# Kernel optimization log

Hardware: AMD Instinct MI355X
Metric: run time of the kernel (lower is better)

Reference implementation:

```python
import jax, jax.numpy as jnp
import numpy as np

B, A, T, H, E, O, TY, SC, AG = 8, 64, 12, 128, 128, 128, 8, 32, 16


def setup_inputs() -> dict:
    ks = jax.random.split(jax.random.key(0), 32)

    def rn(k, shape, s=1.0):
        return jax.random.normal(k, shape, dtype=jnp.float32) * s

    z = lambda *s: jnp.zeros(s, dtype=jnp.float32)
    return {
        "trajectories": rn(ks[0], (B, A, T, 3)),
        "normalized_trajectories": rn(ks[1], (B, A, T, 3)),
        "agent_type": rn(ks[2], (B, A, TY)),
        "scene_data": rn(ks[3], (B, T, SC)),
        "agent_data": rn(ks[4], (B, A, T, AG)),
        "relevant_agents": jnp.ones((B, A), dtype=jnp.float32),
        "W_in": rn(ks[5], (6, H), 0.05), "b_in": z(H),
        "W_node_type": rn(ks[6], (TY, H), 0.05), "b_node_type": z(H),
        "W_agent": rn(ks[7], (AG, H), 0.05), "b_agent": z(H),
        "W_scene": rn(ks[8], (SC, H), 0.05), "b_scene": z(H),
        "W_edge_in": rn(ks[9], (2 * 6 + 2 * TY, E), 0.05), "b_edge_in": z(E),
        "W_edge_type": rn(ks[10], (2 * TY, E), 0.05), "b_edge_type": z(E),
        "W_edge": rn(ks[11], (2 * H + E, E), 0.05), "b_edge": z(E),
        "W_self": rn(ks[12], (H + E + TY, E), 0.05), "b_self": z(E),
        "W_e2n": rn(ks[13], (E, H), 0.05), "b_e2n": z(H),
        "W_ih": rn(ks[14], (5 * H, 4 * H), 0.05),
        "W_hh": rn(ks[15], (H, 4 * H), 0.05),
        "b_ih": z(4 * H), "b_hh": z(4 * H),
        "W_pred": rn(ks[16], (H, O), 0.05), "b_pred": z(O),
    }


def reference(trajectories, normalized_trajectories, agent_type, scene_data, agent_data,
              relevant_agents, W_in, b_in, W_node_type, b_node_type, W_agent, b_agent,
              W_scene, b_scene, W_edge_in, b_edge_in, W_edge_type, b_edge_type,
              W_edge, b_edge, W_self, b_self, W_e2n, b_e2n,
              W_ih, W_hh, b_ih, b_hh, W_pred, b_pred):
    # cat(normalized, raw) along last dim -> 2*(input_dim+1)=6
    both = jnp.concatenate([normalized_trajectories, trajectories], axis=-1)  # [B,A,T,6]
    coord = jax.nn.relu(both @ W_in + b_in)                                   # [B,A,T,H]
    type_enc = agent_type @ W_node_type + b_node_type                          # [B,A,H]
    agent_enc = (agent_data @ W_agent + b_agent) * relevant_agents[:, :, None, None]  # [B,A,T,H]
    scene_enc = scene_data @ W_scene + b_scene                                 # [B,T,H]

    b, a, t_steps = both.shape[0], both.shape[1], both.shape[2]
    Hd = W_in.shape[1]
    Ed = W_edge.shape[1]
    ty = agent_type.shape[-1]

    # initial pairwise edge states from agent features at t=0 + type-pair encoding
    ty_i = jnp.broadcast_to(agent_type[:, :, None, :], (b, a, a, ty))
    ty_j = jnp.broadcast_to(agent_type[:, None, :, :], (b, a, a, ty))
    ty_pair = jnp.concatenate([ty_i, ty_j], axis=-1)                           # [B,A,A,2*TY]
    f0 = both[:, :, 0, :]                                                      # [B,A,6]
    f_i = jnp.broadcast_to(f0[:, :, None, :], (b, a, a, f0.shape[-1]))
    f_j = jnp.broadcast_to(f0[:, None, :, :], (b, a, a, f0.shape[-1]))
    edge0 = (jnp.concatenate([f_i, f_j, ty_pair], axis=-1) @ W_edge_in + b_edge_in
             + ty_pair @ W_edge_type + b_edge_type)                            # [B,A,A,E]

    h0 = jnp.zeros((b, a, Hd), both.dtype)
    c0 = jnp.zeros((b, a, Hd), both.dtype)
    se0 = jnp.zeros((b, a, Ed), both.dtype)

    def step(carry, xs):
        h, c, es, se = carry
        coord_t, scene_t, agent_t, t = xs
        # edge MLP on gathered node pairs (BN is identity in eval, dropout off)
        hi = jnp.broadcast_to(h[:, :, None, :], (b, a, a, Hd))
        hj = jnp.broadcast_to(h[:, None, :, :], (b, a, a, Hd))
        es_new = jnp.concatenate([hi, hj, es], axis=-1) @ W_edge + b_edge      # [B,A,A,E]
        se_new = jnp.concatenate([h, se, agent_type], axis=-1) @ W_self + b_self  # [B,A,E]
        agg = es_new.sum(axis=2) + se_new                                      # scatter-sum to nodes
        node_edges = (agg @ W_e2n + b_e2n) * (t > 0).astype(h.dtype)           # zeros at t==0
        x = jnp.concatenate(
            [coord_t, type_enc, node_edges,
             jnp.broadcast_to(scene_t[:, None, :], (b, a, Hd)), agent_t], axis=-1)  # [B,A,5H]
        gates = x @ W_ih + h @ W_hh + b_ih + b_hh
        gi, gf, gg, go = jnp.split(gates, 4, axis=-1)
        c_new = jax.nn.sigmoid(gf) * c + jax.nn.sigmoid(gi) * jnp.tanh(gg)
        h_new = jax.nn.sigmoid(go) * jnp.tanh(c_new)
        out = jax.nn.relu(h_new @ W_pred + b_pred)                             # layer_pred
        return (h_new, c_new, es_new, se_new), out

    xs = (jnp.moveaxis(coord, 2, 0), jnp.moveaxis(scene_enc, 1, 0),
          jnp.moveaxis(agent_enc, 2, 0), jnp.arange(t_steps))
    _, ys = jax.lax.scan(step, (h0, c0, edge0, se0), xs)                       # ys: [T,B,A,O]
    return jnp.moveaxis(ys, 0, 2)                                              # [B,A,T,O]
```

## Files before the change

kernel.cpp:

```cpp
#include <hip/hip_runtime.h>

constexpr int NB = 8, NA = 64, NT = 12, NH = 128, NTY = 8, NSC = 32, NAG = 16;

struct Params {
    const float *traj, *ntraj, *ty, *sd, *adata, *rel;
    const float *W_in, *b_in, *W_nt, *b_nt, *W_ag, *b_ag, *W_sc, *b_sc;
    const float *W_ein, *b_ein, *W_ety, *b_ety;
    const float *W_edge, *b_edge, *W_self, *b_self, *W_e2n, *b_e2n;
    const float *W_ih, *W_hh, *b_ih, *b_hh, *W_pred, *b_pred;
    float *h0, *h1, *c, *se, *R;
    float *Wty, *Wsc, *Wag, *Wcomb, *vbase, *vag, *vbe, *sesty, *Xs, *hall, *out;
};

__global__ __launch_bounds__(512) void k_fold(Params p) {
    const int blk = blockIdx.x, c = threadIdx.x;
    __shared__ float lrow[NH];
    __shared__ float b1[NH], b2[NH], b3[NH], b4[NH];
    if (blk < 184) {
        const float* src; int ihoff, row; float* dst;
        if (blk < 8)       { row = blk;      src = p.W_nt  + row * NH; ihoff = 128; dst = p.Wty; }
        else if (blk < 40) { row = blk - 8;  src = p.W_sc  + row * NH; ihoff = 384; dst = p.Wsc; }
        else if (blk < 56) { row = blk - 40; src = p.W_ag  + row * NH; ihoff = 512; dst = p.Wag; }
        else               { row = blk - 56; src = p.W_e2n + row * NH; ihoff = 256; dst = p.Wcomb; }
        if (c < NH) lrow[c] = src[c];
        __syncthreads();
        float acc = 0.f;
        for (int k = 0; k < NH; ++k) acc += lrow[k] * p.W_ih[(ihoff + k) * 512 + c];
        dst[row * 512 + c] = acc;
    } else {
        if (c < NH) { b1[c] = p.b_nt[c]; b2[c] = p.b_sc[c]; b3[c] = p.b_ag[c]; b4[c] = p.b_e2n[c]; }
        __syncthreads();
        float vb = p.b_ih[c] + p.b_hh[c], va = 0.f, ve = 0.f;
        for (int k = 0; k < NH; ++k) {
            vb += b1[k] * p.W_ih[(128 + k) * 512 + c] + b2[k] * p.W_ih[(384 + k) * 512 + c];
            va += b3[k] * p.W_ih[(512 + k) * 512 + c];
            ve += b4[k] * p.W_ih[(256 + k) * 512 + c];
        }
        p.vbase[c] = vb; p.vag[c] = va; p.vbe[c] = ve;
    }
}

__global__ void k_r0(Params p) {
    const int row = blockIdx.x, n = threadIdx.x;
    const int b = row / NA, i = row % NA;
    __shared__ float lf[NA][6];
    __shared__ float lt[NA][NTY];
    __shared__ float sumf[6], sumt[NTY];
    if (threadIdx.x < NA) {
        int j = threadIdx.x, rj = b * NA + j;
        for (int k = 0; k < 3; ++k) {
            lf[j][k]     = p.ntraj[(rj * NT + 0) * 3 + k];
            lf[j][3 + k] = p.traj [(rj * NT + 0) * 3 + k];
        }
        for (int k = 0; k < NTY; ++k) lt[j][k] = p.ty[rj * NTY + k];
    }
    __syncthreads();
    if (threadIdx.x < 6) {
        float s = 0.f; for (int j = 0; j < NA; ++j) s += lf[j][threadIdx.x];
        sumf[threadIdx.x] = s;
    } else if (threadIdx.x < 6 + NTY) {
        int k = threadIdx.x - 6; float s = 0.f;
        for (int j = 0; j < NA; ++j) s += lt[j][k];
        sumt[k] = s;
    }
    __syncthreads();
    float acc_i = p.b_ein[n] + p.b_ety[n];
    for (int k = 0; k < 6; ++k)   acc_i += lf[i][k] * p.W_ein[k * NH + n];
    for (int k = 0; k < NTY; ++k) acc_i += lt[i][k] * (p.W_ein[(12 + k) * NH + n] + p.W_ety[k * NH + n]);
    float acc_j = 0.f;
    for (int k = 0; k < 6; ++k)   acc_j += sumf[k] * p.W_ein[(6 + k) * NH + n];
    for (int k = 0; k < NTY; ++k) acc_j += sumt[k] * (p.W_ein[(20 + k) * NH + n] + p.W_ety[(NTY + k) * NH + n]);
    p.R[row * NH + n] = 64.f * acc_i + acc_j;
    float sv = p.b_self[n];
    for (int k = 0; k < NTY; ++k) sv += lt[i][k] * p.W_self[(2 * NH + k) * NH + n];
    p.sesty[row * NH + n] = sv;
}

__global__ __launch_bounds__(512) void k_xstatic(Params p) {
    const int g = blockIdx.x, tid = threadIdx.x, b = g >> 6;
    __shared__ float coordL[NT][NH];
    __shared__ float sceneL[NT][NSC];
    __shared__ float agentL[NT][NAG];
    __shared__ float tyL[NTY];
    const float relv = p.rel[g];
    for (int idx = tid; idx < NT * NH; idx += 512) {
        int r = idx >> 7, k = idx & 127;
        float acc = p.b_in[k];
        const float* nt = p.ntraj + (g * NT + r) * 3;
        const float* tr = p.traj  + (g * NT + r) * 3;
        for (int j = 0; j < 3; ++j) acc += nt[j] * p.W_in[j * NH + k] + tr[j] * p.W_in[(3 + j) * NH + k];
        coordL[r][k] = fmaxf(acc, 0.f);
    }
    for (int i = tid; i < NT * NSC; i += 512) { int r = i >> 5, k = i & 31; sceneL[r][k] = p.sd[(b * NT + r) * NSC + k]; }
    for (int i = tid; i < NT * NAG; i += 512) { int r = i >> 4, k = i & 15; agentL[r][k] = p.adata[(g * NT + r) * NAG + k] * relv; }
    if (tid < NTY) tyL[tid] = p.ty[g * NTY + tid];
    __syncthreads();
    const int c = tid;
    float base = p.vbase[c] + relv * p.vag[c];
    for (int i = 0; i < NTY; ++i) base += tyL[i] * p.Wty[i * 512 + c];
    const float vbeL = p.vbe[c];
    float acc[NT];
#pragma unroll
    for (int r = 0; r < NT; ++r) acc[r] = base + (r > 0 ? vbeL : 0.f);
    for (int k = 0; k < NH; ++k) { float w = p.W_ih[k * 512 + c];
#pragma unroll
        for (int r = 0; r < NT; ++r) acc[r] += coordL[r][k] * w; }
    for (int k = 0; k < NSC; ++k) { float w = p.Wsc[k * 512 + c];
#pragma unroll
        for (int r = 0; r < NT; ++r) acc[r] += sceneL[r][k] * w; }
    for (int k = 0; k < NAG; ++k) { float w = p.Wag[k * 512 + c];
#pragma unroll
        for (int r = 0; r < NT; ++r) acc[r] += agentL[r][k] * w; }
#pragma unroll
    for (int r = 0; r < NT; ++r) p.Xs[((size_t)(g * NT + r)) * 512 + c] = acc[r];
}

__global__ __launch_bounds__(1024) void k_step(Params p, int t) {
    const int tid = threadIdx.x;
    const int r0 = blockIdx.x * 2;
    const int b = r0 >> 6;
    const int n = tid & 127;
    const int g8 = tid >> 7;
    const float* __restrict__ hcur = (t & 1) ? p.h1 : p.h0;
    float* hnxt = (t & 1) ? p.h0 : p.h1;

    __shared__ float lh[2][NH], lR[2][NH], lse[2][NH];
    __shared__ float ps[16][NH];
    __shared__ float hsumL[NH], shw2[NH];
    __shared__ float lagg[2][NH];
    __shared__ float lgp[2][2][512];

    if (tid < 256) {
        int rr = tid >> 7, k = tid & 127;
        lh[rr][k]  = hcur[(r0 + rr) * NH + k];
        lR[rr][k]  = p.R [(r0 + rr) * NH + k];
        lse[rr][k] = p.se[(r0 + rr) * NH + k];
    }
    if (t > 0) {
        float s = 0.f;
        const float* hb = hcur + (b * NA + g8 * 8) * NH + n;
#pragma unroll
        for (int j = 0; j < 8; ++j) s += hb[j * NH];
        ps[g8][n] = s;
    }
    __syncthreads();
    if (t > 0 && tid < NH) {
        float s = 0.f;
#pragma unroll
        for (int q = 0; q < 8; ++q) s += ps[q][tid];
        hsumL[tid] = s;
    }
    __syncthreads();
    if (t > 0) {
        float s = 0.f;
        const float* w2 = p.W_edge + NH * NH + n;
#pragma unroll
        for (int k = 16 * g8; k < 16 * g8 + 16; ++k) s += hsumL[k] * w2[k * NH];
        ps[g8][n] = s;
    }
    __syncthreads();
    if (tid < NH) {
        float s = 0.f;
        if (t > 0) {
#pragma unroll
            for (int q = 0; q < 8; ++q) s += ps[q][tid];
        }
        shw2[tid] = s;
    }
    __syncthreads();

    {
        const int path = g8 >> 1, kh = g8 & 1;
        const float* wb; const float* d0; const float* d1;
        if (path == 0)      { wb = p.W_edge + n;               d0 = lh[0];  d1 = lh[1];  }
        else if (path == 1) { wb = p.W_edge + 2 * NH * NH + n; d0 = lR[0];  d1 = lR[1];  }
        else if (path == 2) { wb = p.W_self + n;               d0 = lh[0];  d1 = lh[1];  }
        else                { wb = p.W_self + NH * NH + n;     d0 = lse[0]; d1 = lse[1]; }
        float a0 = 0.f, a1 = 0.f;
#pragma unroll 8
        for (int k = 64 * kh; k < 64 * kh + 64; ++k) {
            float w = wb[k * NH];
            a0 += d0[k] * w; a1 += d1[k] * w;
        }
        ps[g8 * 2 + 0][n] = a0;
        ps[g8 * 2 + 1][n] = a1;
    }
    __syncthreads();
    if (tid < 256) {
        int rr = tid >> 7, k = tid & 127;
        float a1v = ps[0 + rr][k] + ps[2 + rr][k];
        float a3v = ps[4 + rr][k] + ps[6 + rr][k];
        float aSv = ps[8 + rr][k] + ps[10 + rr][k]
                  + ps[12 + rr][k] + ps[14 + rr][k];
        float Rn = 64.f * a1v + shw2[k] + a3v + 64.f * p.b_edge[k];
        float Sn = aSv + p.sesty[(r0 + rr) * NH + k];
        p.R [(r0 + rr) * NH + k] = Rn;
        p.se[(r0 + rr) * NH + k] = Sn;
        lagg[rr][k] = Rn + Sn;
    }
    __syncthreads();

    {
        const int c = tid & 511, kh2 = tid >> 9;
        float a0 = 0.f, a1v = 0.f;
        if (kh2 == 0) {
            a0  = p.Xs[((size_t)r0 * NT + t) * 512 + c];
            a1v = p.Xs[((size_t)(r0 + 1) * NT + t) * 512 + c];
        }
        if (t > 0) {
            const float* wc = p.Wcomb + c;
            const float* wh = p.W_hh + c;
#pragma unroll 8
            for (int k = 64 * kh2; k < 64 * kh2 + 64; ++k) {
                float w = wc[k * 512];
                a0 += lagg[0][k] * w; a1v += lagg[1][k] * w;
            }
#pragma unroll 8
            for (int k = 64 * kh2; k < 64 * kh2 + 64; ++k) {
                float w = wh[k * 512];
                a0 += lh[0][k] * w; a1v += lh[1][k] * w;
            }
        }
        lgp[kh2][0][c] = a0;
        lgp[kh2][1][c] = a1v;
    }
    __syncthreads();

    if (tid < 256) {
        const int rr = tid >> 7, k = tid & 127, g = r0 + rr;
        float gi = lgp[0][rr][k]          + lgp[1][rr][k];
        float gf = lgp[0][rr][NH + k]     + lgp[1][rr][NH + k];
        float gg = lgp[0][rr][2 * NH + k] + lgp[1][rr][2 * NH + k];
        float go = lgp[0][rr][3 * NH + k] + lgp[1][rr][3 * NH + k];
        float si = 1.f / (1.f + expf(-gi));
        float sf = 1.f / (1.f + expf(-gf));
        float so = 1.f / (1.f + expf(-go));
        float cn = sf * p.c[g * NH + k] + si * tanhf(gg);
        float hn = so * tanhf(cn);
        p.c[g * NH + k] = cn;
        hnxt[g * NH + k] = hn;
        p.hall[((size_t)g * NT + t) * NH + k] = hn;
    }
}

__global__ void k_out(Params p) {
    const int row0 = blockIdx.x * 8, tid = threadIdx.x;
    __shared__ float lhL[8][NH];
    for (int idx = tid; idx < 8 * NH; idx += 256) {
        int r = idx >> 7, k = idx & 127;
        lhL[r][k] = p.hall[((size_t)(row0 + r)) * NH + k];
    }
    __syncthreads();
    const int n = tid & 127, half = tid >> 7, rb = half * 4;
    float a0 = p.b_pred[n], a1 = a0, a2 = a0, a3 = a0;
    for (int k = 0; k < NH; ++k) {
        float w = p.W_pred[k * NH + n];
        a0 += lhL[rb][k] * w; a1 += lhL[rb + 1][k] * w;
        a2 += lhL[rb + 2][k] * w; a3 += lhL[rb + 3][k] * w;
    }
    p.out[((size_t)(row0 + rb))     * NH + n] = fmaxf(a0, 0.f);
    p.out[((size_t)(row0 + rb + 1)) * NH + n] = fmaxf(a1, 0.f);
    p.out[((size_t)(row0 + rb + 2)) * NH + n] = fmaxf(a2, 0.f);
    p.out[((size_t)(row0 + rb + 3)) * NH + n] = fmaxf(a3, 0.f);
}

extern "C" void kernel_launch(void* const* d_in, const int* in_sizes, int n_in,
                              void* d_out, int out_size, void* d_ws, size_t ws_size,
                              hipStream_t stream) {
    const float* const* in = (const float* const*)d_in;
    Params p;
    p.traj = in[0]; p.ntraj = in[1]; p.ty = in[2]; p.sd = in[3]; p.adata = in[4]; p.rel = in[5];
    p.W_in = in[6]; p.b_in = in[7]; p.W_nt = in[8]; p.b_nt = in[9];
    p.W_ag = in[10]; p.b_ag = in[11]; p.W_sc = in[12]; p.b_sc = in[13];
    p.W_ein = in[14]; p.b_ein = in[15]; p.W_ety = in[16]; p.b_ety = in[17];
    p.W_edge = in[18]; p.b_edge = in[19]; p.W_self = in[20]; p.b_self = in[21];
    p.W_e2n = in[22]; p.b_e2n = in[23];
    p.W_ih = in[24]; p.W_hh = in[25]; p.b_ih = in[26]; p.b_hh = in[27];
    p.W_pred = in[28]; p.b_pred = in[29];

    float* ws = (float*)d_ws;
    const size_t S = (size_t)NB * NA * NH;
    p.h0 = ws;
    p.h1 = ws + S;
    p.c  = ws + 2 * S;
    p.se = ws + 3 * S;
    p.R  = ws + 4 * S;
    float* w = ws + 5 * S;
    p.Wty   = w;              w += 8 * 512;
    p.Wsc   = w;              w += 32 * 512;
    p.Wag   = w;              w += 16 * 512;
    p.Wcomb = w;              w += 128 * 512;
    p.vbase = w;              w += 512;
    p.vag   = w;              w += 512;
    p.vbe   = w;              w += 512;
    p.sesty = w;              w += (size_t)NB * NA * NH;
    p.Xs    = w;              w += (size_t)NB * NA * NT * 512;
    p.hall  = w;              w += (size_t)NB * NA * NT * NH;
    p.out = (float*)d_out;

    hipMemsetAsync(p.h0, 0, 4 * S * sizeof(float), stream);
    k_fold<<<185, 512, 0, stream>>>(p);
    k_r0<<<NB * NA, 128, 0, stream>>>(p);
    k_xstatic<<<NB * NA, 512, 0, stream>>>(p);
    for (int t = 0; t < NT; ++t)
        k_step<<<NB * NA / 2, 1024, 0, stream>>>(p, t);
    k_out<<<NB * NA * NT / 8, 256, 0, stream>>>(p);
}
```

Measured before the change: 192.6 us.

## Fuse prelude kernels, process four rows per step block, fold output projection into step

Merges the weight-folding and edge-init kernels into one prelude launch. Each recurrent step block now handles four agent rows instead of two, so each weight load feeds twice as many rows. The prediction layer moves into the step kernel, which removes the hall buffer and the separate output kernel. The cost is half as many step blocks, which means less parallelism across the GPU, plus a longer serial matvec loop per thread.

```diff
diff --git a/kernel.cpp b/kernel.cpp
--- a/kernel.cpp
+++ b/kernel.cpp
@@ -9,71 +9,74 @@
     const float *W_edge, *b_edge, *W_self, *b_self, *W_e2n, *b_e2n;
     const float *W_ih, *W_hh, *b_ih, *b_hh, *W_pred, *b_pred;
     float *h0, *h1, *c, *se, *R;
-    float *Wty, *Wsc, *Wag, *Wcomb, *vbase, *vag, *vbe, *sesty, *Xs, *hall, *out;
+    float *Wty, *Wsc, *Wag, *Wcomb, *vbase, *vag, *vbe, *sesty, *Xs, *out;
 };
 
-__global__ __launch_bounds__(512) void k_fold(Params p) {
-    const int blk = blockIdx.x, c = threadIdx.x;
-    __shared__ float lrow[NH];
-    __shared__ float b1[NH], b2[NH], b3[NH], b4[NH];
-    if (blk < 184) {
-        const float* src; int ihoff, row; float* dst;
-        if (blk < 8)       { row = blk;      src = p.W_nt  + row * NH; ihoff = 128; dst = p.Wty; }
-        else if (blk < 40) { row = blk - 8;  src = p.W_sc  + row * NH; ihoff = 384; dst = p.Wsc; }
-        else if (blk < 56) { row = blk - 40; src = p.W_ag  + row * NH; ihoff = 512; dst = p.Wag; }
-        else               { row = blk - 56; src = p.W_e2n + row * NH; ihoff = 256; dst = p.Wcomb; }
-        if (c < NH) lrow[c] = src[c];
+__global__ __launch_bounds__(512) void k_prelude(Params p) {
+    const int blk = blockIdx.x, tid = threadIdx.x;
+    if (blk < 185) {
+        const int c = tid;
+        __shared__ float lrow[NH];
+        __shared__ float b1[NH], b2[NH], b3[NH], b4[NH];
+        if (blk < 184) {
+            const float* src; int ihoff, row; float* dst;
+            if (blk < 8)       { row = blk;      src = p.W_nt  + row * NH; ihoff = 128; dst = p.Wty; }
+            else if (blk < 40) { row = blk - 8;  src = p.W_sc  + row * NH; ihoff = 384; dst = p.Wsc; }
+            else if (blk < 56) { row = blk - 40; src = p.W_ag  + row * NH; ihoff = 512; dst = p.Wag; }
+            else               { row = blk - 56; src = p.W_e2n + row * NH; ihoff = 256; dst = p.Wcomb; }
+            if (c < NH) lrow[c] = src[c];
+            __syncthreads();
+            float acc = 0.f;
+            for (int k = 0; k < NH; ++k) acc += lrow[k] * p.W_ih[(ihoff + k) * 512 + c];
+            dst[row * 512 + c] = acc;
+        } else {
+            if (c < NH) { b1[c] = p.b_nt[c]; b2[c] = p.b_sc[c]; b3[c] = p.b_ag[c]; b4[c] = p.b_e2n[c]; }
+            __syncthreads();
+            float vb = p.b_ih[c] + p.b_hh[c], va = 0.f, ve = 0.f;
+            for (int k = 0; k < NH; ++k) {
+                vb += b1[k] * p.W_ih[(128 + k) * 512 + c] + b2[k] * p.W_ih[(384 + k) * 512 + c];
+                va += b3[k] * p.W_ih[(512 + k) * 512 + c];
+                ve += b4[k] * p.W_ih[(256 + k) * 512 + c];
+            }
+            p.vbase[c] = vb; p.vag[c] = va; p.vbe[c] = ve;
+        }
+    } else {
+        const int r0g = (blk - 185) * 4;
+        const int b = r0g >> 6;
+        const int q = tid >> 7, n = tid & 127;
+        const int row = r0g + q, i = row & 63;
+        __shared__ float lf[NA][6];
+        __shared__ float lt[NA][NTY];
+        __shared__ float sumf[6], sumt[NTY];
+        if (tid < NA) {
+            int j = tid, rj = b * NA + j;
+            for (int k = 0; k < 3; ++k) {
+                lf[j][k]     = p.ntraj[(rj * NT + 0) * 3 + k];
+                lf[j][3 + k] = p.traj [(rj * NT + 0) * 3 + k];
+            }
+            for (int k = 0; k < NTY; ++k) lt[j][k] = p.ty[rj * NTY + k];
+        }
         __syncthreads();
-        float acc = 0.f;
-        for (int k = 0; k < NH; ++k) acc += lrow[k] * p.W_ih[(ihoff + k) * 512 + c];
-        dst[row * 512 + c] = acc;
-    } else {
-        if (c < NH) { b1[c] = p.b_nt[c]; b2[c] = p.b_sc[c]; b3[c] = p.b_ag[c]; b4[c] = p.b_e2n[c]; }
+        if (tid < 6) {
+            float s = 0.f; for (int j = 0; j < NA; ++j) s += lf[j][tid];
+            sumf[tid] = s;
+        } else if (tid < 6 + NTY) {
+            int k = tid - 6; float s = 0.f;
+            for (int j = 0; j < NA; ++j) s += lt[j][k];
+            sumt[k] = s;
+        }
         __syncthreads();
-        float vb = p.b_ih[c] + p.b_hh[c], va = 0.f, ve = 0.f;
-        for (int k = 0; k < NH; ++k) {
-            vb += b1[k] * p.W_ih[(128 + k) * 512 + c] + b2[k] * p.W_ih[(384 + k) * 512 + c];
-            va += b3[k] * p.W_ih[(512 + k) * 512 + c];
-            ve += b4[k] * p.W_ih[(256 + k) * 512 + c];
-        }
-        p.vbase[c] = vb; p.vag[c] = va; p.vbe[c] = ve;
-    }
-}
-
-__global__ void k_r0(Params p) {
-    const int row = blockIdx.x, n = threadIdx.x;
-    const int b = row / NA, i = row % NA;
-    __shared__ float lf[NA][6];
-    __shared__ float lt[NA][NTY];
-    __shared__ float sumf[6], sumt[NTY];
-    if (threadIdx.x < NA) {
-        int j = threadIdx.x, rj = b * NA + j;
-        for (int k = 0; k < 3; ++k) {
-            lf[j][k]     = p.ntraj[(rj * NT + 0) * 3 + k];
-            lf[j][3 + k] = p.traj [(rj * NT + 0) * 3 + k];
-        }
-        for (int k = 0; k < NTY; ++k) lt[j][k] = p.ty[rj * NTY + k];
-    }
-    __syncthreads();
-    if (threadIdx.x < 6) {
-        float s = 0.f; for (int j = 0; j < NA; ++j) s += lf[j][threadIdx.x];
-        sumf[threadIdx.x] = s;
-    } else if (threadIdx.x < 6 + NTY) {
-        int k = threadIdx.x - 6; float s = 0.f;
-        for (int j = 0; j < NA; ++j) s += lt[j][k];
-        sumt[k] = s;
-    }
-    __syncthreads();
-    float acc_i = p.b_ein[n] + p.b_ety[n];
-    for (int k = 0; k < 6; ++k)   acc_i += lf[i][k] * p.W_ein[k * NH + n];
-    for (int k = 0; k < NTY; ++k) acc_i += lt[i][k] * (p.W_ein[(12 + k) * NH + n] + p.W_ety[k * NH + n]);
-    float acc_j = 0.f;
-    for (int k = 0; k < 6; ++k)   acc_j += sumf[k] * p.W_ein[(6 + k) * NH + n];
-    for (int k = 0; k < NTY; ++k) acc_j += sumt[k] * (p.W_ein[(20 + k) * NH + n] + p.W_ety[(NTY + k) * NH + n]);
-    p.R[row * NH + n] = 64.f * acc_i + acc_j;
-    float sv = p.b_self[n];
-    for (int k = 0; k < NTY; ++k) sv += lt[i][k] * p.W_self[(2 * NH + k) * NH + n];
-    p.sesty[row * NH + n] = sv;
+        float acc_i = p.b_ein[n] + p.b_ety[n];
+        for (int k = 0; k < 6; ++k)   acc_i += lf[i][k] * p.W_ein[k * NH + n];
+        for (int k = 0; k < NTY; ++k) acc_i += lt[i][k] * (p.W_ein[(12 + k) * NH + n] + p.W_ety[k * NH + n]);
+        float acc_j = 0.f;
+        for (int k = 0; k < 6; ++k)   acc_j += sumf[k] * p.W_ein[(6 + k) * NH + n];
+        for (int k = 0; k < NTY; ++k) acc_j += sumt[k] * (p.W_ein[(20 + k) * NH + n] + p.W_ety[(NTY + k) * NH + n]);
+        p.R[row * NH + n] = 64.f * acc_i + acc_j;
+        float sv = p.b_self[n];
+        for (int k = 0; k < NTY; ++k) sv += lt[i][k] * p.W_self[(2 * NH + k) * NH + n];
+        p.sesty[row * NH + n] = sv;
+    }
 }
 
 __global__ __launch_bounds__(512) void k_xstatic(Params p) {
@@ -117,20 +120,20 @@
 
 __global__ __launch_bounds__(1024) void k_step(Params p, int t) {
     const int tid = threadIdx.x;
-    const int r0 = blockIdx.x * 2;
+    const int r0 = blockIdx.x * 4;
     const int b = r0 >> 6;
     const int n = tid & 127;
     const int g8 = tid >> 7;
     const float* __restrict__ hcur = (t & 1) ? p.h1 : p.h0;
     float* hnxt = (t & 1) ? p.h0 : p.h1;
 
-    __shared__ float lh[2][NH], lR[2][NH], lse[2][NH];
+    __shared__ float lh[4][NH], lR[4][NH], lse[4][NH];
     __shared__ float ps[16][NH];
     __shared__ float hsumL[NH], shw2[NH];
-    __shared__ float lagg[2][NH];
-    __shared__ float lgp[2][2][512];
-
-    if (tid < 256) {
+    __shared__ float lagg[4][NH];
+    __shared__ float lgp[2][4][512];
+
+    if (tid < 512) {
         int rr = tid >> 7, k = tid & 127;
         lh[rr][k]  = hcur[(r0 + rr) * NH + k];
         lR[rr][k]  = p.R [(r0 + rr) * NH + k];
@@ -170,28 +173,27 @@
     __syncthreads();
 
     {
-        const int path = g8 >> 1, kh = g8 & 1;
+        const int path = g8 >> 1, rp = g8 & 1;
         const float* wb; const float* d0; const float* d1;
-        if (path == 0)      { wb = p.W_edge + n;               d0 = lh[0];  d1 = lh[1];  }
-        else if (path == 1) { wb = p.W_edge + 2 * NH * NH + n; d0 = lR[0];  d1 = lR[1];  }
-        else if (path == 2) { wb = p.W_self + n;               d0 = lh[0];  d1 = lh[1];  }
-        else                { wb = p.W_self + NH * NH + n;     d0 = lse[0]; d1 = lse[1]; }
+        if (path == 0)      { wb = p.W_edge + n;               d0 = lh[2 * rp];  d1 = lh[2 * rp + 1];  }
+        else if (path == 1) { wb = p.W_edge + 2 * NH * NH + n; d0 = lR[2 * rp];  d1 = lR[2 * rp + 1];  }
+        else if (path == 2) { wb = p.W_self + n;               d0 = lh[2 * rp];  d1 = lh[2 * rp + 1];  }
+        else                { wb = p.W_self + NH * NH + n;     d0 = lse[2 * rp]; d1 = lse[2 * rp + 1]; }
         float a0 = 0.f, a1 = 0.f;
 #pragma unroll 8
-        for (int k = 64 * kh; k < 64 * kh + 64; ++k) {
+        for (int k = 0; k < NH; ++k) {
             float w = wb[k * NH];
             a0 += d0[k] * w; a1 += d1[k] * w;
         }
-        ps[g8 * 2 + 0][n] = a0;
-        ps[g8 * 2 + 1][n] = a1;
-    }
-    __syncthreads();
-    if (tid < 256) {
+        ps[path * 4 + 2 * rp + 0][n] = a0;
+        ps[path * 4 + 2 * rp + 1][n] = a1;
+    }
+    __syncthreads();
+    if (tid < 512) {
         int rr = tid >> 7, k = tid & 127;
-        float a1v = ps[0 + rr][k] + ps[2 + rr][k];
-        float a3v = ps[4 + rr][k] + ps[6 + rr][k];
-        float aSv = ps[8 + rr][k] + ps[10 + rr][k]
-                  + ps[12 + rr][k] + ps[14 + rr][k];
+        float a1v = ps[0 + rr][k];
+        float a3v = ps[4 + rr][k];
+        float aSv = ps[8 + rr][k] + ps[12 + rr][k];
         float Rn = 64.f * a1v + shw2[k] + a3v + 64.f * p.b_edge[k];
         float Sn = aSv + p.sesty[(r0 + rr) * NH + k];
         p.R [(r0 + rr) * NH + k] = Rn;
@@ -201,32 +203,36 @@
     __syncthreads();
 
     {
-        const int c = tid & 511, kh2 = tid >> 9;
-        float a0 = 0.f, a1v = 0.f;
-        if (kh2 == 0) {
-            a0  = p.Xs[((size_t)r0 * NT + t) * 512 + c];
-            a1v = p.Xs[((size_t)(r0 + 1) * NT + t) * 512 + c];
+        const int c = tid & 511, kh = tid >> 9;
+        float a0 = 0.f, a1 = 0.f, a2 = 0.f, a3 = 0.f;
+        if (kh == 0) {
+            a0 = p.Xs[((size_t)(r0 + 0) * NT + t) * 512 + c];
+            a1 = p.Xs[((size_t)(r0 + 1) * NT + t) * 512 + c];
+            a2 = p.Xs[((size_t)(r0 + 2) * NT + t) * 512 + c];
+            a3 = p.Xs[((size_t)(r0 + 3) * NT + t) * 512 + c];
         }
         if (t > 0) {
             const float* wc = p.Wcomb + c;
             const float* wh = p.W_hh + c;
 #pragma unroll 8
-            for (int k = 64 * kh2; k < 64 * kh2 + 64; ++k) {
+            for (int k = 64 * kh; k < 64 * kh + 64; ++k) {
                 float w = wc[k * 512];
-                a0 += lagg[0][k] * w; a1v += lagg[1][k] * w;
+                a0 += lagg[0][k] * w; a1 += lagg[1][k] * w;
+                a2 += lagg[2][k] * w; a3 += lagg[3][k] * w;
             }
 #pragma unroll 8
-            for (int k = 64 * kh2; k < 64 * kh2 + 64; ++k) {
+            for (int k = 64 * kh; k < 64 * kh + 64; ++k) {
                 float w = wh[k * 512];
-                a0 += lh[0][k] * w; a1v += lh[1][k] * w;
+                a0 += lh[0][k] * w; a1 += lh[1][k] * w;
+                a2 += lh[2][k] * w; a3 += lh[3][k] * w;
             }
         }
-        lgp[kh2][0][c] = a0;
-        lgp[kh2][1][c] = a1v;
-    }
-    __syncthreads();
-
-    if (tid < 256) {
+        lgp[kh][0][c] = a0; lgp[kh][1][c] = a1;
+        lgp[kh][2][c] = a2; lgp[kh][3][c] = a3;
+    }
+    __syncthreads();
+
+    if (tid < 512) {
         const int rr = tid >> 7, k = tid & 127, g = r0 + rr;
         float gi = lgp[0][rr][k]          + lgp[1][rr][k];
         float gf = lgp[0][rr][NH + k]     + lgp[1][rr][NH + k];
@@ -239,29 +245,24 @@
         float hn = so * tanhf(cn);
         p.c[g * NH + k] = cn;
         hnxt[g * NH + k] = hn;
-        p.hall[((size_t)g * NT + t) * NH + k] = hn;
-    }
-}
-
-__global__ void k_out(Params p) {
-    const int row0 = blockIdx.x * 8, tid = threadIdx.x;
-    __shared__ float lhL[8][NH];
-    for (int idx = tid; idx < 8 * NH; idx += 256) {
-        int r = idx >> 7, k = idx & 127;
-        lhL[r][k] = p.hall[((size_t)(row0 + r)) * NH + k];
-    }
-    __syncthreads();
-    const int n = tid & 127, half = tid >> 7, rb = half * 4;
-    float a0 = p.b_pred[n], a1 = a0, a2 = a0, a3 = a0;
-    for (int k = 0; k < NH; ++k) {
-        float w = p.W_pred[k * NH + n];
-        a0 += lhL[rb][k] * w; a1 += lhL[rb + 1][k] * w;
-        a2 += lhL[rb + 2][k] * w; a3 += lhL[rb + 3][k] * w;
-    }
-    p.out[((size_t)(row0 + rb))     * NH + n] = fmaxf(a0, 0.f);
-    p.out[((size_t)(row0 + rb + 1)) * NH + n] = fmaxf(a1, 0.f);
-    p.out[((size_t)(row0 + rb + 2)) * NH + n] = fmaxf(a2, 0.f);
-    p.out[((size_t)(row0 + rb + 3)) * NH + n] = fmaxf(a3, 0.f);
+        lh[rr][k] = hn;
+    }
+    __syncthreads();
+
+    {
+        const int q = (tid >> 7) & 3, kh = tid >> 9;
+        float s = 0.f;
+        const float* wp = p.W_pred + n;
+#pragma unroll 8
+        for (int k = 64 * kh; k < 64 * kh + 64; ++k) s += lh[q][k] * wp[k * NH];
+        ps[kh * 4 + q][n] = s;
+    }
+    __syncthreads();
+    if (tid < 512) {
+        const int q = tid >> 7, k = tid & 127;
+        float v = ps[q][k] + ps[4 + q][k] + p.b_pred[k];
+        p.out[((size_t)(r0 + q) * NT + t) * NH + k] = fmaxf(v, 0.f);
+    }
 }
 
 extern "C" void kernel_launch(void* const* d_in, const int* in_sizes, int n_in,
@@ -295,14 +296,11 @@
     p.vbe   = w;              w += 512;
     p.sesty = w;              w += (size_t)NB * NA * NH;
     p.Xs    = w;              w += (size_t)NB * NA * NT * 512;
-    p.hall  = w;              w += (size_t)NB * NA * NT * NH;
     p.out = (float*)d_out;
 
     hipMemsetAsync(p.h0, 0, 4 * S * sizeof(float), stream);
-    k_fold<<<185, 512, 0, stream>>>(p);
-    k_r0<<<NB * NA, 128, 0, stream>>>(p);
+    k_prelude<<<313, 512, 0, stream>>>(p);
     k_xstatic<<<NB * NA, 512, 0, stream>>>(p);
     for (int t = 0; t < NT; ++t)
-        k_step<<<NB * NA / 2, 1024, 0, stream>>>(p, t);
-    k_out<<<NB * NA * NT / 8, 256, 0, stream>>>(p);
+        k_step<<<NB * NA / 4, 1024, 0, stream>>>(p, t);
 }
```

After: 251.4 us. +30.5%, slower.

## Fuse prelude kernels, fold output projection into step, trim step barriers

Applied to the files above, without the earlier changes.

Merges the memset, weight-folding kernel and R0 kernel into one prelude launch, with extra blocks handling four rows each and zeroing state inline. Moves the output projection (W_pred + ReLU) into the per-timestep kernel, removing the hall buffer and the separate output launch. Also merges the neighbour-sum reduction into the W_edge matvec, which drops two barriers from each step. The step kernel gains a W_pred matvec and two barriers per timestep, which lengthens the serial critical path.

```diff
diff --git a/kernel.cpp b/kernel.cpp
--- a/kernel.cpp
+++ b/kernel.cpp
@@ -9,71 +9,77 @@
     const float *W_edge, *b_edge, *W_self, *b_self, *W_e2n, *b_e2n;
     const float *W_ih, *W_hh, *b_ih, *b_hh, *W_pred, *b_pred;
     float *h0, *h1, *c, *se, *R;
-    float *Wty, *Wsc, *Wag, *Wcomb, *vbase, *vag, *vbe, *sesty, *Xs, *hall, *out;
+    float *Wty, *Wsc, *Wag, *Wcomb, *vbase, *vag, *vbe, *sesty, *Xs, *out;
 };
 
-__global__ __launch_bounds__(512) void k_fold(Params p) {
-    const int blk = blockIdx.x, c = threadIdx.x;
-    __shared__ float lrow[NH];
-    __shared__ float b1[NH], b2[NH], b3[NH], b4[NH];
-    if (blk < 184) {
-        const float* src; int ihoff, row; float* dst;
-        if (blk < 8)       { row = blk;      src = p.W_nt  + row * NH; ihoff = 128; dst = p.Wty; }
-        else if (blk < 40) { row = blk - 8;  src = p.W_sc  + row * NH; ihoff = 384; dst = p.Wsc; }
-        else if (blk < 56) { row = blk - 40; src = p.W_ag  + row * NH; ihoff = 512; dst = p.Wag; }
-        else               { row = blk - 56; src = p.W_e2n + row * NH; ihoff = 256; dst = p.Wcomb; }
-        if (c < NH) lrow[c] = src[c];
+__global__ __launch_bounds__(512) void k_prelude(Params p) {
+    const int blk = blockIdx.x, tid = threadIdx.x;
+    if (blk < 185) {
+        const int c = tid;
+        __shared__ float lrow[NH];
+        __shared__ float b1[NH], b2[NH], b3[NH], b4[NH];
+        if (blk < 184) {
+            const float* src; int ihoff, row; float* dst;
+            if (blk < 8)       { row = blk;      src = p.W_nt  + row * NH; ihoff = 128; dst = p.Wty; }
+            else if (blk < 40) { row = blk - 8;  src = p.W_sc  + row * NH; ihoff = 384; dst = p.Wsc; }
+            else if (blk < 56) { row = blk - 40; src = p.W_ag  + row * NH; ihoff = 512; dst = p.Wag; }
+            else               { row = blk - 56; src = p.W_e2n + row * NH; ihoff = 256; dst = p.Wcomb; }
+            if (c < NH) lrow[c] = src[c];
+            __syncthreads();
+            float acc = 0.f;
+            for (int k = 0; k < NH; ++k) acc += lrow[k] * p.W_ih[(ihoff + k) * 512 + c];
+            dst[row * 512 + c] = acc;
+        } else {
+            if (c < NH) { b1[c] = p.b_nt[c]; b2[c] = p.b_sc[c]; b3[c] = p.b_ag[c]; b4[c] = p.b_e2n[c]; }
+            __syncthreads();
+            float vb = p.b_ih[c] + p.b_hh[c], va = 0.f, ve = 0.f;
+            for (int k = 0; k < NH; ++k) {
+                vb += b1[k] * p.W_ih[(128 + k) * 512 + c] + b2[k] * p.W_ih[(384 + k) * 512 + c];
+                va += b3[k] * p.W_ih[(512 + k) * 512 + c];
+                ve += b4[k] * p.W_ih[(256 + k) * 512 + c];
+            }
+            p.vbase[c] = vb; p.vag[c] = va; p.vbe[c] = ve;
+        }
+    } else {
+        const int r0g = (blk - 185) * 4;
+        const int b = r0g >> 6;
+        const int q = tid >> 7, n = tid & 127;
+        const int row = r0g + q, i = row & 63;
+        __shared__ float lf[NA][6];
+        __shared__ float lt[NA][NTY];
+        __shared__ float sumf[6], sumt[NTY];
+        if (tid < NA) {
+            int j = tid, rj = b * NA + j;
+            for (int k = 0; k < 3; ++k) {
+                lf[j][k]     = p.ntraj[(rj * NT + 0) * 3 + k];
+                lf[j][3 + k] = p.traj [(rj * NT + 0) * 3 + k];
+            }
+            for (int k = 0; k < NTY; ++k) lt[j][k] = p.ty[rj * NTY + k];
+        }
+        p.h0[row * NH + n] = 0.f;
+        p.c [row * NH + n] = 0.f;
+        p.se[row * NH + n] = 0.f;
         __syncthreads();
-        float acc = 0.f;
-        for (int k = 0; k < NH; ++k) acc += lrow[k] * p.W_ih[(ihoff + k) * 512 + c];
-        dst[row * 512 + c] = acc;
-    } else {
-        if (c < NH) { b1[c] = p.b_nt[c]; b2[c] = p.b_sc[c]; b3[c] = p.b_ag[c]; b4[c] = p.b_e2n[c]; }
+        if (tid < 6) {
+            float s = 0.f; for (int j = 0; j < NA; ++j) s += lf[j][tid];
+            sumf[tid] = s;
+        } else if (tid < 6 + NTY) {
+            int k = tid - 6; float s = 0.f;
+            for (int j = 0; j < NA; ++j) s += lt[j][k];
+            sumt[k] = s;
+        }
         __syncthreads();
-        float vb = p.b_ih[c] + p.b_hh[c], va = 0.f, ve = 0.f;
-        for (int k = 0; k < NH; ++k) {
-            vb += b1[k] * p.W_ih[(128 + k) * 512 + c] + b2[k] * p.W_ih[(384 + k) * 512 + c];
-            va += b3[k] * p.W_ih[(512 + k) * 512 + c];
-            ve += b4[k] * p.W_ih[(256 + k) * 512 + c];
-        }
-        p.vbase[c] = vb; p.vag[c] = va; p.vbe[c] = ve;
-    }
-}
-
-__global__ void k_r0(Params p) {
-    const int row = blockIdx.x, n = threadIdx.x;
-    const int b = row / NA, i = row % NA;
-    __shared__ float lf[NA][6];
-    __shared__ float lt[NA][NTY];
-    __shared__ float sumf[6], sumt[NTY];
-    if (threadIdx.x < NA) {
-        int j = threadIdx.x, rj = b * NA + j;
-        for (int k = 0; k < 3; ++k) {
-            lf[j][k]     = p.ntraj[(rj * NT + 0) * 3 + k];
-            lf[j][3 + k] = p.traj [(rj * NT + 0) * 3 + k];
-        }
-        for (int k = 0; k < NTY; ++k) lt[j][k] = p.ty[rj * NTY + k];
-    }
-    __syncthreads();
-    if (threadIdx.x < 6) {
-        float s = 0.f; for (int j = 0; j < NA; ++j) s += lf[j][threadIdx.x];
-        sumf[threadIdx.x] = s;
-    } else if (threadIdx.x < 6 + NTY) {
-        int k = threadIdx.x - 6; float s = 0.f;
-        for (int j = 0; j < NA; ++j) s += lt[j][k];
-        sumt[k] = s;
-    }
-    __syncthreads();
-    float acc_i = p.b_ein[n] + p.b_ety[n];
-    for (int k = 0; k < 6; ++k)   acc_i += lf[i][k] * p.W_ein[k * NH + n];
-    for (int k = 0; k < NTY; ++k) acc_i += lt[i][k] * (p.W_ein[(12 + k) * NH + n] + p.W_ety[k * NH + n]);
-    float acc_j = 0.f;
-    for (int k = 0; k < 6; ++k)   acc_j += sumf[k] * p.W_ein[(6 + k) * NH + n];
-    for (int k = 0; k < NTY; ++k) acc_j += sumt[k] * (p.W_ein[(20 + k) * NH + n] + p.W_ety[(NTY + k) * NH + n]);
-    p.R[row * NH + n] = 64.f * acc_i + acc_j;
-    float sv = p.b_self[n];
-    for (int k = 0; k < NTY; ++k) sv += lt[i][k] * p.W_self[(2 * NH + k) * NH + n];
-    p.sesty[row * NH + n] = sv;
+        float acc_i = p.b_ein[n] + p.b_ety[n];
+        for (int k = 0; k < 6; ++k)   acc_i += lf[i][k] * p.W_ein[k * NH + n];
+        for (int k = 0; k < NTY; ++k) acc_i += lt[i][k] * (p.W_ein[(12 + k) * NH + n] + p.W_ety[k * NH + n]);
+        float acc_j = 0.f;
+        for (int k = 0; k < 6; ++k)   acc_j += sumf[k] * p.W_ein[(6 + k) * NH + n];
+        for (int k = 0; k < NTY; ++k) acc_j += sumt[k] * (p.W_ein[(20 + k) * NH + n] + p.W_ety[(NTY + k) * NH + n]);
+        p.R[row * NH + n] = 64.f * acc_i + acc_j;
+        float sv = p.b_self[n];
+        for (int k = 0; k < NTY; ++k) sv += lt[i][k] * p.W_self[(2 * NH + k) * NH + n];
+        p.sesty[row * NH + n] = sv;
+    }
 }
 
 __global__ __launch_bounds__(512) void k_xstatic(Params p) {
@@ -125,8 +131,9 @@
     float* hnxt = (t & 1) ? p.h0 : p.h1;
 
     __shared__ float lh[2][NH], lR[2][NH], lse[2][NH];
+    __shared__ float psum[8][NH];
+    __shared__ float ps2[8][NH];
     __shared__ float ps[16][NH];
-    __shared__ float hsumL[NH], shw2[NH];
     __shared__ float lagg[2][NH];
     __shared__ float lgp[2][2][512];
 
@@ -141,34 +148,21 @@
         const float* hb = hcur + (b * NA + g8 * 8) * NH + n;
 #pragma unroll
         for (int j = 0; j < 8; ++j) s += hb[j * NH];
-        ps[g8][n] = s;
-    }
-    __syncthreads();
-    if (t > 0 && tid < NH) {
-        float s = 0.f;
-#pragma unroll
-        for (int q = 0; q < 8; ++q) s += ps[q][tid];
-        hsumL[tid] = s;
-    }
-    __syncthreads();
+        psum[g8][n] = s;
+    }
+    __syncthreads();
+
     if (t > 0) {
         float s = 0.f;
         const float* w2 = p.W_edge + NH * NH + n;
 #pragma unroll
-        for (int k = 16 * g8; k < 16 * g8 + 16; ++k) s += hsumL[k] * w2[k * NH];
-        ps[g8][n] = s;
-    }
-    __syncthreads();
-    if (tid < NH) {
-        float s = 0.f;
-        if (t > 0) {
-#pragma unroll
-            for (int q = 0; q < 8; ++q) s += ps[q][tid];
-        }
-        shw2[tid] = s;
-    }
-    __syncthreads();
-
+        for (int k = 16 * g8; k < 16 * g8 + 16; ++k) {
+            float hv = psum[0][k] + psum[1][k] + psum[2][k] + psum[3][k]
+                     + psum[4][k] + psum[5][k] + psum[6][k] + psum[7][k];
+            s += hv * w2[k * NH];
+        }
+        ps2[g8][n] = s;
+    }
     {
         const int path = g8 >> 1, kh = g8 & 1;
         const float* wb; const float* d0; const float* d1;
@@ -186,13 +180,19 @@
         ps[g8 * 2 + 1][n] = a1;
     }
     __syncthreads();
+
     if (tid < 256) {
         int rr = tid >> 7, k = tid & 127;
+        float shw2v = 0.f;
+        if (t > 0) {
+#pragma unroll
+            for (int q = 0; q < 8; ++q) shw2v += ps2[q][k];
+        }
         float a1v = ps[0 + rr][k] + ps[2 + rr][k];
         float a3v = ps[4 + rr][k] + ps[6 + rr][k];
         float aSv = ps[8 + rr][k] + ps[10 + rr][k]
                   + ps[12 + rr][k] + ps[14 + rr][k];
-        float Rn = 64.f * a1v + shw2[k] + a3v + 64.f * p.b_edge[k];
+        float Rn = 64.f * a1v + shw2v + a3v + 64.f * p.b_edge[k];
         float Sn = aSv + p.sesty[(r0 + rr) * NH + k];
         p.R [(r0 + rr) * NH + k] = Rn;
         p.se[(r0 + rr) * NH + k] = Sn;
@@ -239,29 +239,24 @@
         float hn = so * tanhf(cn);
         p.c[g * NH + k] = cn;
         hnxt[g * NH + k] = hn;
-        p.hall[((size_t)g * NT + t) * NH + k] = hn;
-    }
-}
-
-__global__ void k_out(Params p) {
-    const int row0 = blockIdx.x * 8, tid = threadIdx.x;
-    __shared__ float lhL[8][NH];
-    for (int idx = tid; idx < 8 * NH; idx += 256) {
-        int r = idx >> 7, k = idx & 127;
-        lhL[r][k] = p.hall[((size_t)(row0 + r)) * NH + k];
-    }
-    __syncthreads();
-    const int n = tid & 127, half = tid >> 7, rb = half * 4;
-    float a0 = p.b_pred[n], a1 = a0, a2 = a0, a3 = a0;
-    for (int k = 0; k < NH; ++k) {
-        float w = p.W_pred[k * NH + n];
-        a0 += lhL[rb][k] * w; a1 += lhL[rb + 1][k] * w;
-        a2 += lhL[rb + 2][k] * w; a3 += lhL[rb + 3][k] * w;
-    }
-    p.out[((size_t)(row0 + rb))     * NH + n] = fmaxf(a0, 0.f);
-    p.out[((size_t)(row0 + rb + 1)) * NH + n] = fmaxf(a1, 0.f);
-    p.out[((size_t)(row0 + rb + 2)) * NH + n] = fmaxf(a2, 0.f);
-    p.out[((size_t)(row0 + rb + 3)) * NH + n] = fmaxf(a3, 0.f);
+        lh[rr][k] = hn;
+    }
+    __syncthreads();
+
+    {
+        const int r = g8 & 1, kq = g8 >> 1;
+        float s = 0.f;
+        const float* wp = p.W_pred + n;
+#pragma unroll
+        for (int k = 32 * kq; k < 32 * kq + 32; ++k) s += lh[r][k] * wp[k * NH];
+        ps[g8][n] = s;
+    }
+    __syncthreads();
+    if (tid < 256) {
+        const int rr = tid >> 7, k = tid & 127;
+        float v = ps[rr][k] + ps[2 + rr][k] + ps[4 + rr][k] + ps[6 + rr][k] + p.b_pred[k];
+        p.out[((size_t)(r0 + rr) * NT + t) * NH + k] = fmaxf(v, 0.f);
+    }
 }
 
 extern "C" void kernel_launch(void* const* d_in, const int* in_sizes, int n_in,
@@ -295,14 +290,10 @@
     p.vbe   = w;              w += 512;
     p.sesty = w;              w += (size_t)NB * NA * NH;
     p.Xs    = w;              w += (size_t)NB * NA * NT * 512;
-    p.hall  = w;              w += (size_t)NB * NA * NT * NH;
     p.out = (float*)d_out;
 
-    hipMemsetAsync(p.h0, 0, 4 * S * sizeof(float), stream);
-    k_fold<<<185, 512, 0, stream>>>(p);
-    k_r0<<<NB * NA, 128, 0, stream>>>(p);
+    k_prelude<<<313, 512, 0, stream>>>(p);
     k_xstatic<<<NB * NA, 512, 0, stream>>>(p);
     for (int t = 0; t < NT; ++t)
         k_step<<<NB * NA / 2, 1024, 0, stream>>>(p, t);
-    k_out<<<NB * NA * NT / 8, 256, 0, stream>>>(p);
-}
+}
```

Measured after the change: 191.5 us. About the same (-0.6%).
